# Kernel tuning notes

Hardware: AMD Instinct MI355X
Metric: run time of the kernel (lower is better)

Reference implementation:

```python
import jax, jax.numpy as jnp
import numpy as np

D_MODEL = 1024
NUM_HEADS = 16
HEAD_SIZE = D_MODEL // NUM_HEADS
THETA = 10000.0
MAX_SEQ_LEN = 4096


def _rope_tables():
    # (max_seq_len, head_size//2) cos/sin tables, matching RotaryPositionalEmbedding
    k = jnp.arange(HEAD_SIZE // 2, dtype=jnp.float32)
    inv_freq = 1.0 / (THETA ** (2.0 * k / HEAD_SIZE))
    pos = jnp.arange(MAX_SEQ_LEN, dtype=jnp.float32)
    ang = pos[:, None] * inv_freq[None, :]
    return jnp.cos(ang), jnp.sin(ang)


def _apply_rope(x, cos, sin):
    # x: (b, h, s, d); cos/sin: (s, d//2) -> broadcast over (b, h)
    x1 = x[..., ::2]
    x2 = x[..., 1::2]
    out_even = x1 * cos - x2 * sin
    out_odd = x2 * cos + x1 * sin
    # re-interleave pairs back to (..., d)
    return jnp.stack([out_even, out_odd], axis=-1).reshape(x.shape)


def setup_inputs() -> dict:
    key = jax.random.key(0)
    k1, k2, k3 = jax.random.split(key, 3)
    b, s = 1, 4096
    std_qkv = np.sqrt(2.0 / (D_MODEL + 3 * D_MODEL))
    std_o = np.sqrt(2.0 / (D_MODEL + D_MODEL))
    return {
        "x": jax.random.normal(k1, (b, s, D_MODEL), dtype=jnp.float32),
        "token_positions": jnp.arange(s, dtype=jnp.int32),
        "W_qkv": jax.random.normal(k2, (3 * D_MODEL, D_MODEL), dtype=jnp.float32) * std_qkv,
        "W_o": jax.random.normal(k3, (D_MODEL, D_MODEL), dtype=jnp.float32) * std_o,
    }


def reference(x, token_positions, W_qkv, W_o):
    b, s, _ = x.shape
    qkv = jnp.einsum("bsd,ed->bse", x, W_qkv)  # (b, s, 3*d_model)
    q, k, v = jnp.split(qkv, 3, axis=-1)

    def to_heads(t):
        return t.reshape(b, s, NUM_HEADS, HEAD_SIZE).transpose(0, 2, 1, 3)  # (b, h, s, hs)

    q, k, v = to_heads(q), to_heads(k), to_heads(v)

    cos_tab, sin_tab = _rope_tables()
    cos = cos_tab[token_positions]  # (s, hs//2)
    sin = sin_tab[token_positions]
    q = _apply_rope(q, cos, sin)
    k = _apply_rope(k, cos, sin)

    scale = 1.0 / jnp.sqrt(jnp.asarray(HEAD_SIZE, dtype=x.dtype))
    scores = jnp.einsum("bhqd,bhkd->bhqk", q, k) * scale  # (b, h, s, s)
    causal = jnp.tril(jnp.ones((s, s), dtype=bool))
    scores = jnp.where(causal, scores, jnp.finfo(scores.dtype).min)
    attn = jax.nn.softmax(scores, axis=-1)
    out = jnp.einsum("bhqk,bhkd->bhqd", attn, v)  # (b, h, s, hs)
    out = out.transpose(0, 2, 1, 3).reshape(b, s, D_MODEL)
    return jnp.einsum("bsd,ed->bse", out, W_o)
```

## Files before the change

kernel.cpp:

```cpp
#include <hip/hip_runtime.h>
#include <stdint.h>

typedef unsigned short u16;
typedef __attribute__((ext_vector_type(8))) short bf16x8;
typedef __attribute__((ext_vector_type(4))) float f32x4;

#define LN_THETA 9.210340371976184f
#define SLEN 4096
#define DMODEL 1024

__device__ __forceinline__ u16 f2bf(float f) {
  union { float f; unsigned u; } v; v.f = f;
  unsigned u = v.u;
  return (u16)((u + 0x7FFFu + ((u >> 16) & 1u)) >> 16);
}
__device__ __forceinline__ u16 f2bf_trunc(float f) {
  union { float f; unsigned u; } v; v.f = f;
  return (u16)(v.u >> 16);
}
__device__ __forceinline__ float bf2f(u16 b) {
  union { unsigned u; float f; } v; v.u = ((unsigned)b) << 16;
  return v.f;
}

__device__ __forceinline__ f32x4 mfma16(bf16x8 a, bf16x8 b, f32x4 c) {
  return __builtin_amdgcn_mfma_f32_16x16x32_bf16(a, b, c, 0, 0, 0);
}

__device__ __forceinline__ void async16(const u16* g, u16* l) {
  __builtin_amdgcn_global_load_lds(
      (const __attribute__((address_space(1))) unsigned int*)g,
      (__attribute__((address_space(3))) unsigned int*)l, 16, 0, 0);
}

__global__ void rope_tab_kernel(const int* __restrict__ tokpos,
                                float2* __restrict__ tab) {
  int t = blockIdx.x * 256 + threadIdx.x;
  int s = t >> 5, i = t & 31;
  float inv = expf(-(float)(2 * i) * (LN_THETA / 64.0f));
  float ang = (float)tokpos[s] * inv;
  float sn, cs;
  sincosf(ang, &sn, &cs);
  tab[t] = make_float2(cs, sn);
}

__global__ void cvt_all_kernel(const float* __restrict__ x,
                               const float* __restrict__ wqkv,
                               const float* __restrict__ wo,
                               u16* __restrict__ xb, u16* __restrict__ wqkvb,
                               u16* __restrict__ wob) {
  int i = blockIdx.x * 256 + threadIdx.x;
  const float* src;
  u16* dst;
  if (i < (1 << 20)) {
    src = x; dst = xb;
  } else if (i < (1 << 20) + (3 << 18)) {
    i -= (1 << 20); src = wqkv; dst = wqkvb;
  } else {
    i -= (1 << 20) + (3 << 18); src = wo; dst = wob;
  }
  float4 v = ((const float4*)src)[i];
  ushort4 o;
  o.x = f2bf(v.x); o.y = f2bf(v.y); o.z = f2bf(v.z); o.w = f2bf(v.w);
  ((ushort4*)dst)[i] = o;
}

__global__ __launch_bounds__(256) void gemm_qkv_kernel(
    const u16* __restrict__ A, const u16* __restrict__ B,
    u16* __restrict__ qb, u16* __restrict__ kb,
    u16* __restrict__ vbT, const float2* __restrict__ cstab) {
  const int K = 1024;
  __shared__ __align__(16) u16 As[128][32];
  __shared__ __align__(16) u16 Bs[128][32];
  __shared__ __align__(16) u16 Ts[128][136];
  const int tid = threadIdx.x;
  const int wave = tid >> 6, lane = tid & 63;
  const int quad = lane >> 4, col = lane & 15;
  const int rowBase = blockIdx.x * 128;
  const int colBase = blockIdx.y * 128;
  const int wm = (wave >> 1) * 64, wn = (wave & 1) * 64;

  const int sRow = wave * 32 + (lane >> 2);
  const int sK = (lane & 3) * 8;
  const u16* gA = A + (size_t)(rowBase + sRow) * K + sK;
  const u16* gB = B + (size_t)(colBase + sRow) * K + sK;

  f32x4 acc[4][4];
#pragma unroll
  for (int i = 0; i < 4; ++i)
#pragma unroll
    for (int j = 0; j < 4; ++j)
      acc[i][j] = f32x4{0.f, 0.f, 0.f, 0.f};

  for (int kk = 0; kk < K; kk += 32) {
    __syncthreads();
    async16(gA + kk, &As[sRow][sK]);
    async16(gA + kk + 16 * K, &As[sRow + 16][sK]);
    async16(gB + kk, &Bs[sRow][sK]);
    async16(gB + kk + 16 * K, &Bs[sRow + 16][sK]);
    __syncthreads();
    bf16x8 af[4], bfr[4];
#pragma unroll
    for (int i = 0; i < 4; ++i)
      af[i] = *(const bf16x8*)&As[wm + i * 16 + col][quad * 8];
#pragma unroll
    for (int j = 0; j < 4; ++j)
      bfr[j] = *(const bf16x8*)&Bs[wn + j * 16 + col][quad * 8];
#pragma unroll
    for (int i = 0; i < 4; ++i)
#pragma unroll
      for (int j = 0; j < 4; ++j)
        acc[i][j] = mfma16(af[i], bfr[j], acc[i][j]);
  }

  const int sec = rowBase >> 10;

  if (sec < 2) {
#pragma unroll
    for (int j = 0; j < 4; ++j) {
      int sl = wn + j * 16 + col;
      int s = colBase + sl;
#pragma unroll
      for (int i = 0; i < 4; ++i) {
        int el = wm + i * 16 + quad * 4;
        int d = (rowBase + el) & 63;
        float v0 = acc[i][j][0], v1 = acc[i][j][1];
        float v2 = acc[i][j][2], v3 = acc[i][j][3];
        float2 cs0 = cstab[s * 32 + (d >> 1)];
        float2 cs1 = cstab[s * 32 + (d >> 1) + 1];
        ushort4 pk;
        pk.x = f2bf(v0 * cs0.x - v1 * cs0.y);
        pk.y = f2bf(v1 * cs0.x + v0 * cs0.y);
        pk.z = f2bf(v2 * cs1.x - v3 * cs1.y);
        pk.w = f2bf(v3 * cs1.x + v2 * cs1.y);
        *(ushort4*)&Ts[sl][el] = pk;
      }
    }
    __syncthreads();
    int sl = tid >> 1, hf = tid & 1;
    int hh = ((rowBase & 1023) >> 6) + hf;
    u16* dst = (sec == 0 ? qb : kb) + ((size_t)hh * SLEN + colBase + sl) * 64;
    const u16* srcp = &Ts[sl][hf * 64];
#pragma unroll
    for (int kq = 0; kq < 8; ++kq)
      ((int4*)dst)[kq] = ((const int4*)srcp)[kq];
  } else {
#pragma unroll
    for (int j = 0; j < 4; ++j) {
      int sl = wn + j * 16 + col;
#pragma unroll
      for (int i = 0; i < 4; ++i) {
        int el = wm + i * 16 + quad * 4;
#pragma unroll
        for (int r = 0; r < 4; ++r)
          Ts[el + r][sl] = f2bf(acc[i][j][r]);
      }
    }
    __syncthreads();
    int el = tid >> 1, sh = tid & 1;
    int e = rowBase - 2048 + el;
    int hh = e >> 6, d = e & 63;
    u16* dst = vbT + (size_t)(hh * 64 + d) * SLEN + colBase + sh * 64;
    const u16* srcp = &Ts[el][sh * 64];
#pragma unroll
    for (int kq = 0; kq < 8; ++kq)
      ((int4*)dst)[kq] = ((const int4*)srcp)[kq];
  }
}

__global__ __launch_bounds__(256) void gemm_out_kernel(
    const u16* __restrict__ A, const u16* __restrict__ B,
    float* __restrict__ outf) {
  const int K = 1024;
  __shared__ __align__(16) u16 As[128][32];
  __shared__ __align__(16) u16 Bs[64][32];
  const int tid = threadIdx.x;
  const int wave = tid >> 6, lane = tid & 63;
  const int quad = lane >> 4, col = lane & 15;
  const int rowBase = blockIdx.x * 128;
  const int colBase = blockIdx.y * 64;

  const int sRow = wave * 32 + (lane >> 2);
  const int bRow = wave * 16 + (lane >> 2);
  const int sK = (lane & 3) * 8;
  const u16* gA = A + (size_t)(rowBase + sRow) * K + sK;
  const u16* gB = B + (size_t)(colBase + bRow) * K + sK;

  f32x4 acc[2][4];
#pragma unroll
  for (int i = 0; i < 2; ++i)
#pragma unroll
    for (int j = 0; j < 4; ++j)
      acc[i][j] = f32x4{0.f, 0.f, 0.f, 0.f};

  for (int kk = 0; kk < K; kk += 32) {
    __syncthreads();
    async16(gA + kk, &As[sRow][sK]);
    async16(gA + kk + 16 * K, &As[sRow + 16][sK]);
    async16(gB + kk, &Bs[bRow][sK]);
    __syncthreads();
    bf16x8 af[2], bfr[4];
#pragma unroll
    for (int i = 0; i < 2; ++i)
      af[i] = *(const bf16x8*)&As[wave * 32 + i * 16 + col][quad * 8];
#pragma unroll
    for (int j = 0; j < 4; ++j)
      bfr[j] = *(const bf16x8*)&Bs[j * 16 + col][quad * 8];
#pragma unroll
    for (int i = 0; i < 2; ++i)
#pragma unroll
      for (int j = 0; j < 4; ++j)
        acc[i][j] = mfma16(af[i], bfr[j], acc[i][j]);
  }

#pragma unroll
  for (int i = 0; i < 2; ++i) {
    int r0 = rowBase + wave * 32 + i * 16 + quad * 4;
#pragma unroll
    for (int j = 0; j < 4; ++j) {
      int cc = colBase + j * 16 + col;
#pragma unroll
      for (int r = 0; r < 4; ++r)
        outf[(size_t)(r0 + r) * DMODEL + cc] = acc[i][j][r];
    }
  }
}

__global__ __launch_bounds__(128) void flash_kernel(
    const u16* __restrict__ qbuf, const u16* __restrict__ kbuf,
    const u16* __restrict__ vbT, u16* __restrict__ po,
    float* __restrict__ pl) {
  const int S = SLEN;
  const int h = blockIdx.x;
  const int y = blockIdx.y;
  int tile, c0, c1;
  if (y < 32) {
    tile = 32 + y; c0 = 0; c1 = 31;
  } else {
    int k = (y - 32) >> 1;
    if ((y - 32) & 1) { tile = 31 - k; c0 = 0; c1 = tile; }
    else { tile = 63 - k; c0 = 32; c1 = tile; }
  }
  const int id = (tile < 32) ? tile : (32 + 2 * (tile - 32) + (c0 ? 1 : 0));

  const int wave = threadIdx.x >> 6, lane = threadIdx.x & 63;
  const int quad = lane >> 4, col = lane & 15;
  const u16* Q = qbuf + (size_t)h * S * 64;
  const u16* Kh = kbuf + (size_t)h * S * 64;
  const u16* Vt = vbT + (size_t)h * 64 * S;

  __shared__ __align__(16) u16 Ks[64][64];
  __shared__ __align__(16) u16 Vs[64][64];
  __shared__ __align__(16) u16 Pld[2][2][16][72];

  const int sr = lane >> 3;
  const int sw = ((lane & 7) ^ sr) * 8;
  const int dcol = (lane & 7) * 8;
  const int segA = ((quad ^ (col & 7)) * 8);
  const int segB = (((quad ^ 4) ^ (col & 7)) * 8);

  const int qrow0 = tile * 64 + wave * 32;

  bf16x8 qf0[2], qf1[2];
#pragma unroll
  for (int i = 0; i < 2; ++i) {
    const u16* qp = &Q[(size_t)(qrow0 + i * 16 + col) * 64 + quad * 8];
    qf0[i] = *(const bf16x8*)qp;
    qf1[i] = *(const bf16x8*)(qp + 32);
  }

  f32x4 o[2][4];
#pragma unroll
  for (int i = 0; i < 2; ++i)
#pragma unroll
    for (int n = 0; n < 4; ++n) o[i][n] = f32x4{0.f, 0.f, 0.f, 0.f};
  float lrow[2][4] = {{0.f, 0.f, 0.f, 0.f}, {0.f, 0.f, 0.f, 0.f}};

  for (int c = c0; c <= c1; ++c) {
    const int k0 = c * 64;
    __syncthreads();
    {
#pragma unroll
      for (int t = 0; t < 4; ++t) {
        int row = (t * 2 + wave) * 8 + sr;
        async16(Kh + (size_t)(k0 + row) * 64 + sw, &Ks[row][dcol]);
        async16(Vt + (size_t)row * S + k0 + sw, &Vs[row][dcol]);
      }
    }
    __syncthreads();

    bf16x8 kf0[4], kf1[4], vf0[4], vf1[4];
#pragma unroll
    for (int j = 0; j < 4; ++j) {
      kf0[j] = *(const bf16x8*)&Ks[16 * j + col][segA];
      kf1[j] = *(const bf16x8*)&Ks[16 * j + col][segB];
    }
#pragma unroll
    for (int n = 0; n < 4; ++n) {
      vf0[n] = *(const bf16x8*)&Vs[16 * n + col][segA];
      vf1[n] = *(const bf16x8*)&Vs[16 * n + col][segB];
    }
    const bool lastc = (c == tile);
#pragma unroll
    for (int i = 0; i < 2; ++i) {
      f32x4 s[4];
#pragma unroll
      for (int j = 0; j < 4; ++j)
        s[j] = mfma16(qf1[i], kf1[j],
                      mfma16(qf0[i], kf0[j], f32x4{0.f, 0.f, 0.f, 0.f}));
      float p[4][4];
#pragma unroll
      for (int r = 0; r < 4; ++r) {
        const int qrel = wave * 32 + i * 16 + quad * 4 + r;
#pragma unroll
        for (int j = 0; j < 4; ++j) {
          float e = __expf(s[j][r] * 0.125f);
          if (lastc && (16 * j + col > qrel)) e = 0.f;
          p[j][r] = e;
        }
        lrow[i][r] += (p[0][r] + p[1][r]) + (p[2][r] + p[3][r]);
      }
#pragma unroll
      for (int j = 0; j < 4; ++j)
#pragma unroll
        for (int r = 0; r < 4; ++r)
          Pld[wave][i][quad * 4 + r][16 * j + col] = f2bf_trunc(p[j][r]);
      bf16x8 pa0 = *(const bf16x8*)&Pld[wave][i][col][quad * 8];
      bf16x8 pa1 = *(const bf16x8*)&Pld[wave][i][col][quad * 8 + 32];
#pragma unroll
      for (int n = 0; n < 4; ++n)
        o[i][n] = mfma16(pa1, vf1[n], mfma16(pa0, vf0[n], o[i][n]));
    }
  }

  u16* pob = po + (((size_t)h * 96 + id) * 64) * 64;
  float* plb = pl + ((size_t)h * 96 + id) * 64;
#pragma unroll
  for (int i = 0; i < 2; ++i) {
#pragma unroll
    for (int m = 1; m <= 8; m <<= 1)
#pragma unroll
      for (int r = 0; r < 4; ++r) lrow[i][r] += __shfl_xor(lrow[i][r], m);
#pragma unroll
    for (int r = 0; r < 4; ++r) {
      int rowl = wave * 32 + i * 16 + quad * 4 + r;
      u16* dst = pob + (size_t)rowl * 64 + col;
#pragma unroll
      for (int n = 0; n < 4; ++n) dst[16 * n] = f2bf(o[i][n][r]);
      if (col == 0) plb[rowl] = lrow[i][r];
    }
  }
}

__global__ __launch_bounds__(256) void reduce_kernel(
    const u16* __restrict__ po, const float* __restrict__ pl,
    u16* __restrict__ attn) {
  const int h = blockIdx.x, tile = blockIdx.y;
  const int tid = threadIdx.x;
  const int row = tid >> 2, dg = (tid & 3) * 16;
  int id0, ns;
  if (tile < 32) { id0 = tile; ns = 1; }
  else { id0 = 32 + 2 * (tile - 32); ns = 2; }

  float acc[16];
#pragma unroll
  for (int q = 0; q < 16; ++q) acc[q] = 0.f;
  float l = 0.f;
  for (int s = 0; s < ns; ++s) {
    const size_t base = ((size_t)h * 96 + id0 + s) * 64;
    const u16* p = po + (base + row) * 64 + dg;
    l += pl[base + row];
#pragma unroll
    for (int q = 0; q < 16; ++q) acc[q] += bf2f(p[q]);
  }
  float inv = 1.0f / l;
  u16* dst = attn + (size_t)(tile * 64 + row) * DMODEL + h * 64 + dg;
  ushort4 o0, o1, o2, o3;
  o0.x = f2bf(acc[0] * inv);  o0.y = f2bf(acc[1] * inv);
  o0.z = f2bf(acc[2] * inv);  o0.w = f2bf(acc[3] * inv);
  o1.x = f2bf(acc[4] * inv);  o1.y = f2bf(acc[5] * inv);
  o1.z = f2bf(acc[6] * inv);  o1.w = f2bf(acc[7] * inv);
  o2.x = f2bf(acc[8] * inv);  o2.y = f2bf(acc[9] * inv);
  o2.z = f2bf(acc[10] * inv); o2.w = f2bf(acc[11] * inv);
  o3.x = f2bf(acc[12] * inv); o3.y = f2bf(acc[13] * inv);
  o3.z = f2bf(acc[14] * inv); o3.w = f2bf(acc[15] * inv);
  ((ushort4*)dst)[0] = o0; ((ushort4*)dst)[1] = o1;
  ((ushort4*)dst)[2] = o2; ((ushort4*)dst)[3] = o3;
}

extern "C" void kernel_launch(void* const* d_in, const int* in_sizes, int n_in,
                              void* d_out, int out_size, void* d_ws,
                              size_t ws_size, hipStream_t stream) {
  const float* x = (const float*)d_in[0];
  const int* tokpos = (const int*)d_in[1];
  const float* wqkv = (const float*)d_in[2];
  const float* wo = (const float*)d_in[3];
  float* out = (float*)d_out;

  char* ws = (char*)d_ws;
  u16* xb    = (u16*)(ws);
  u16* wqkvb = (u16*)(ws + ((size_t)8 << 20));
  u16* wob   = (u16*)(ws + ((size_t)14 << 20));
  u16* qb    = (u16*)(ws + ((size_t)16 << 20));
  u16* kb    = (u16*)(ws + ((size_t)24 << 20));
  u16* vbT   = (u16*)(ws + ((size_t)32 << 20));
  u16* attn  = (u16*)(ws + ((size_t)40 << 20));
  float2* cstab = (float2*)(ws + ((size_t)48 << 20));
  u16* po    = (u16*)(ws);
  float* pl  = (float*)(ws + ((size_t)13 << 20));

  rope_tab_kernel<<<dim3(512), dim3(256), 0, stream>>>(tokpos, cstab);
  cvt_all_kernel<<<dim3(8192), dim3(256), 0, stream>>>(x, wqkv, wo, xb, wqkvb,
                                                       wob);
  gemm_qkv_kernel<<<dim3(24, 32), dim3(256), 0, stream>>>(
      wqkvb, xb, qb, kb, vbT, cstab);
  flash_kernel<<<dim3(16, 96), dim3(128), 0, stream>>>(qb, kb, vbT, po, pl);
  reduce_kernel<<<dim3(16, 64), dim3(256), 0, stream>>>(po, pl, attn);
  gemm_out_kernel<<<dim3(32, 16), dim3(256), 0, stream>>>(attn, wob, out);
}
```

Measured before the change: 232.5 us.

## Widen GEMM K-tiles with swizzled LDS, fold softmax scale into Q, MFMA row sums

Both projection GEMMs now stage 64-wide K slices per barrier pair, using an XOR-swizzled LDS layout, and the QKV kernel aliases its transpose buffer onto the A/B tiles to save shared memory. The 1/sqrt(d) scale is folded into Q during the RoPE epilogue, which removes a multiply per score in the flash loop. Softmax row sums are now computed with an MFMA against a ones vector on the bf16-truncated P instead of VALU adds and shuffles. The aim is to halve GEMM barrier overhead and remove VALU and shuffle work from the attention inner loop. The row sums now come from truncated bf16 values, and Q carries an extra rounding step after scaling.

```diff
diff --git a/kernel.cpp b/kernel.cpp
--- a/kernel.cpp
+++ b/kernel.cpp
@@ -70,9 +70,10 @@
     u16* __restrict__ qb, u16* __restrict__ kb,
     u16* __restrict__ vbT, const float2* __restrict__ cstab) {
   const int K = 1024;
-  __shared__ __align__(16) u16 As[128][32];
-  __shared__ __align__(16) u16 Bs[128][32];
-  __shared__ __align__(16) u16 Ts[128][136];
+  __shared__ __align__(16) char smem[128 * 136 * 2];
+  u16 (*As)[64] = (u16(*)[64])smem;
+  u16 (*Bs)[64] = (u16(*)[64])(smem + 16384);
+  u16 (*Ts)[136] = (u16(*)[136])smem;
   const int tid = threadIdx.x;
   const int wave = tid >> 6, lane = tid & 63;
   const int quad = lane >> 4, col = lane & 15;
@@ -80,10 +81,14 @@
   const int colBase = blockIdx.y * 128;
   const int wm = (wave >> 1) * 64, wn = (wave & 1) * 64;
 
-  const int sRow = wave * 32 + (lane >> 2);
-  const int sK = (lane & 3) * 8;
-  const u16* gA = A + (size_t)(rowBase + sRow) * K + sK;
-  const u16* gB = B + (size_t)(colBase + sRow) * K + sK;
+  const int sr8 = lane >> 3;
+  const int sseg = ((lane & 7) ^ sr8) * 8;
+  const u16* gA = A + (size_t)(rowBase + wave * 8 + sr8) * K + sseg;
+  const u16* gB = B + (size_t)(colBase + wave * 8 + sr8) * K + sseg;
+  u16* ldsA = &As[wave * 8 + sr8][(lane & 7) * 8];
+  u16* ldsB = &Bs[wave * 8 + sr8][(lane & 7) * 8];
+
+  const int segh[2] = {((quad ^ (col & 7)) * 8), (((4 + quad) ^ (col & 7)) * 8)};
 
   f32x4 acc[4][4];
 #pragma unroll
@@ -92,30 +97,36 @@
     for (int j = 0; j < 4; ++j)
       acc[i][j] = f32x4{0.f, 0.f, 0.f, 0.f};
 
-  for (int kk = 0; kk < K; kk += 32) {
-    __syncthreads();
-    async16(gA + kk, &As[sRow][sK]);
-    async16(gA + kk + 16 * K, &As[sRow + 16][sK]);
-    async16(gB + kk, &Bs[sRow][sK]);
-    async16(gB + kk + 16 * K, &Bs[sRow + 16][sK]);
-    __syncthreads();
-    bf16x8 af[4], bfr[4];
-#pragma unroll
-    for (int i = 0; i < 4; ++i)
-      af[i] = *(const bf16x8*)&As[wm + i * 16 + col][quad * 8];
-#pragma unroll
-    for (int j = 0; j < 4; ++j)
-      bfr[j] = *(const bf16x8*)&Bs[wn + j * 16 + col][quad * 8];
-#pragma unroll
-    for (int i = 0; i < 4; ++i)
+  for (int kk = 0; kk < K; kk += 64) {
+    __syncthreads();
+#pragma unroll
+    for (int j = 0; j < 4; ++j) {
+      async16(gA + (size_t)j * 32 * K + kk, ldsA + j * 32 * 64);
+      async16(gB + (size_t)j * 32 * K + kk, ldsB + j * 32 * 64);
+    }
+    __syncthreads();
+#pragma unroll
+    for (int h = 0; h < 2; ++h) {
+      bf16x8 af[4], bfr[4];
+#pragma unroll
+      for (int i = 0; i < 4; ++i)
+        af[i] = *(const bf16x8*)&As[wm + i * 16 + col][segh[h]];
 #pragma unroll
       for (int j = 0; j < 4; ++j)
-        acc[i][j] = mfma16(af[i], bfr[j], acc[i][j]);
-  }
+        bfr[j] = *(const bf16x8*)&Bs[wn + j * 16 + col][segh[h]];
+#pragma unroll
+      for (int i = 0; i < 4; ++i)
+#pragma unroll
+        for (int j = 0; j < 4; ++j)
+          acc[i][j] = mfma16(af[i], bfr[j], acc[i][j]);
+    }
+  }
+  __syncthreads();
 
   const int sec = rowBase >> 10;
 
   if (sec < 2) {
+    const float qs = (sec == 0) ? 0.125f : 1.0f;
 #pragma unroll
     for (int j = 0; j < 4; ++j) {
       int sl = wn + j * 16 + col;
@@ -129,10 +140,10 @@
         float2 cs0 = cstab[s * 32 + (d >> 1)];
         float2 cs1 = cstab[s * 32 + (d >> 1) + 1];
         ushort4 pk;
-        pk.x = f2bf(v0 * cs0.x - v1 * cs0.y);
-        pk.y = f2bf(v1 * cs0.x + v0 * cs0.y);
-        pk.z = f2bf(v2 * cs1.x - v3 * cs1.y);
-        pk.w = f2bf(v3 * cs1.x + v2 * cs1.y);
+        pk.x = f2bf(qs * (v0 * cs0.x - v1 * cs0.y));
+        pk.y = f2bf(qs * (v1 * cs0.x + v0 * cs0.y));
+        pk.z = f2bf(qs * (v2 * cs1.x - v3 * cs1.y));
+        pk.w = f2bf(qs * (v3 * cs1.x + v2 * cs1.y));
         *(ushort4*)&Ts[sl][el] = pk;
       }
     }
@@ -172,19 +183,22 @@
     const u16* __restrict__ A, const u16* __restrict__ B,
     float* __restrict__ outf) {
   const int K = 1024;
-  __shared__ __align__(16) u16 As[128][32];
-  __shared__ __align__(16) u16 Bs[64][32];
+  __shared__ __align__(16) u16 As[128][64];
+  __shared__ __align__(16) u16 Bs[64][64];
   const int tid = threadIdx.x;
   const int wave = tid >> 6, lane = tid & 63;
   const int quad = lane >> 4, col = lane & 15;
   const int rowBase = blockIdx.x * 128;
   const int colBase = blockIdx.y * 64;
 
-  const int sRow = wave * 32 + (lane >> 2);
-  const int bRow = wave * 16 + (lane >> 2);
-  const int sK = (lane & 3) * 8;
-  const u16* gA = A + (size_t)(rowBase + sRow) * K + sK;
-  const u16* gB = B + (size_t)(colBase + bRow) * K + sK;
+  const int sr8 = lane >> 3;
+  const int sseg = ((lane & 7) ^ sr8) * 8;
+  const u16* gA = A + (size_t)(rowBase + wave * 8 + sr8) * K + sseg;
+  const u16* gB = B + (size_t)(colBase + wave * 8 + sr8) * K + sseg;
+  u16* ldsA = &As[wave * 8 + sr8][(lane & 7) * 8];
+  u16* ldsB = &Bs[wave * 8 + sr8][(lane & 7) * 8];
+
+  const int segh[2] = {((quad ^ (col & 7)) * 8), (((4 + quad) ^ (col & 7)) * 8)};
 
   f32x4 acc[2][4];
 #pragma unroll
@@ -193,24 +207,30 @@
     for (int j = 0; j < 4; ++j)
       acc[i][j] = f32x4{0.f, 0.f, 0.f, 0.f};
 
-  for (int kk = 0; kk < K; kk += 32) {
-    __syncthreads();
-    async16(gA + kk, &As[sRow][sK]);
-    async16(gA + kk + 16 * K, &As[sRow + 16][sK]);
-    async16(gB + kk, &Bs[bRow][sK]);
-    __syncthreads();
-    bf16x8 af[2], bfr[4];
-#pragma unroll
-    for (int i = 0; i < 2; ++i)
-      af[i] = *(const bf16x8*)&As[wave * 32 + i * 16 + col][quad * 8];
+  for (int kk = 0; kk < K; kk += 64) {
+    __syncthreads();
 #pragma unroll
     for (int j = 0; j < 4; ++j)
-      bfr[j] = *(const bf16x8*)&Bs[j * 16 + col][quad * 8];
-#pragma unroll
-    for (int i = 0; i < 2; ++i)
+      async16(gA + (size_t)j * 32 * K + kk, ldsA + j * 32 * 64);
+#pragma unroll
+    for (int j = 0; j < 2; ++j)
+      async16(gB + (size_t)j * 32 * K + kk, ldsB + j * 32 * 64);
+    __syncthreads();
+#pragma unroll
+    for (int h = 0; h < 2; ++h) {
+      bf16x8 af[2], bfr[4];
+#pragma unroll
+      for (int i = 0; i < 2; ++i)
+        af[i] = *(const bf16x8*)&As[wave * 32 + i * 16 + col][segh[h]];
 #pragma unroll
       for (int j = 0; j < 4; ++j)
-        acc[i][j] = mfma16(af[i], bfr[j], acc[i][j]);
+        bfr[j] = *(const bf16x8*)&Bs[j * 16 + col][segh[h]];
+#pragma unroll
+      for (int i = 0; i < 2; ++i)
+#pragma unroll
+        for (int j = 0; j < 4; ++j)
+          acc[i][j] = mfma16(af[i], bfr[j], acc[i][j]);
+    }
   }
 
 #pragma unroll
@@ -269,12 +289,17 @@
     qf1[i] = *(const bf16x8*)(qp + 32);
   }
 
-  f32x4 o[2][4];
-#pragma unroll
-  for (int i = 0; i < 2; ++i)
+  const bf16x8 ones = {(short)0x3F80, (short)0x3F80, (short)0x3F80,
+                       (short)0x3F80, (short)0x3F80, (short)0x3F80,
+                       (short)0x3F80, (short)0x3F80};
+
+  f32x4 o[2][4], lacc[2];
+#pragma unroll
+  for (int i = 0; i < 2; ++i) {
 #pragma unroll
     for (int n = 0; n < 4; ++n) o[i][n] = f32x4{0.f, 0.f, 0.f, 0.f};
-  float lrow[2][4] = {{0.f, 0.f, 0.f, 0.f}, {0.f, 0.f, 0.f, 0.f}};
+    lacc[i] = f32x4{0.f, 0.f, 0.f, 0.f};
+  }
 
   for (int c = c0; c <= c1; ++c) {
     const int k0 = c * 64;
@@ -314,11 +339,10 @@
         const int qrel = wave * 32 + i * 16 + quad * 4 + r;
 #pragma unroll
         for (int j = 0; j < 4; ++j) {
-          float e = __expf(s[j][r] * 0.125f);
+          float e = __expf(s[j][r]);
           if (lastc && (16 * j + col > qrel)) e = 0.f;
           p[j][r] = e;
         }
-        lrow[i][r] += (p[0][r] + p[1][r]) + (p[2][r] + p[3][r]);
       }
 #pragma unroll
       for (int j = 0; j < 4; ++j)
@@ -327,6 +351,7 @@
           Pld[wave][i][quad * 4 + r][16 * j + col] = f2bf_trunc(p[j][r]);
       bf16x8 pa0 = *(const bf16x8*)&Pld[wave][i][col][quad * 8];
       bf16x8 pa1 = *(const bf16x8*)&Pld[wave][i][col][quad * 8 + 32];
+      lacc[i] = mfma16(pa1, ones, mfma16(pa0, ones, lacc[i]));
 #pragma unroll
       for (int n = 0; n < 4; ++n)
         o[i][n] = mfma16(pa1, vf1[n], mfma16(pa0, vf0[n], o[i][n]));
@@ -337,17 +362,13 @@
   float* plb = pl + ((size_t)h * 96 + id) * 64;
 #pragma unroll
   for (int i = 0; i < 2; ++i) {
-#pragma unroll
-    for (int m = 1; m <= 8; m <<= 1)
-#pragma unroll
-      for (int r = 0; r < 4; ++r) lrow[i][r] += __shfl_xor(lrow[i][r], m);
 #pragma unroll
     for (int r = 0; r < 4; ++r) {
       int rowl = wave * 32 + i * 16 + quad * 4 + r;
       u16* dst = pob + (size_t)rowl * 64 + col;
 #pragma unroll
       for (int n = 0; n < 4; ++n) dst[16 * n] = f2bf(o[i][n][r]);
-      if (col == 0) plb[rowl] = lrow[i][r];
+      if (col == 0) plb[rowl] = lacc[i][r];
     }
   }
 }
```

Result: faster. 220.2 us (-5.3%).
